# Kernel tuning notes

Hardware: AMD Instinct MI355X
Metric: run time of the kernel (lower is better)

The kernel has to match this reference:

```python
import jax, jax.numpy as jnp
import numpy as np

NUM_INPUTS = 1024
NUM_HIDDEN = 1024
FORGET_GATE_BIAS = -1.0
EPS = 1e-5


def layer_norm_1d(x, weight, bias):
    # Matches torch LayerNorm1D: std is unbiased (ddof=1), divide by (std + eps)
    mean = jnp.mean(x, axis=1, keepdims=True)
    std = jnp.std(x, axis=1, keepdims=True, ddof=1)
    return (x - mean) / (std + EPS) * weight + bias


def setup_inputs() -> dict:
    key = jax.random.key(0)
    ks = jax.random.split(key, 8)
    B, I, H = 4096, NUM_INPUTS, NUM_HIDDEN
    lim_i = 1.0 / np.sqrt(I)
    lim_h = 1.0 / np.sqrt(H)
    return {
        "inputs": jax.random.normal(ks[0], (B, I), jnp.float32),
        "hx": jax.random.normal(ks[1], (B, H), jnp.float32),
        "cx": jax.random.normal(ks[2], (B, H), jnp.float32),
        "w_i2h": jax.random.uniform(ks[3], (4 * H, I), jnp.float32, -lim_i, lim_i),
        "b_i2h": jax.random.uniform(ks[4], (4 * H,), jnp.float32, -lim_i, lim_i),
        "w_h2h": jax.random.uniform(ks[5], (4 * H, H), jnp.float32, -lim_h, lim_h),
        "b_h2h": jax.random.uniform(ks[6], (4 * H,), jnp.float32, -lim_h, lim_h),
        "ln_i2h_w": jnp.ones((1, 4 * H), jnp.float32),
        "ln_i2h_b": jnp.zeros((1, 4 * H), jnp.float32),
        "ln_h2h_w": jnp.ones((1, 4 * H), jnp.float32),
        "ln_h2h_b": jnp.zeros((1, 4 * H), jnp.float32),
        "ln_h2o_w": jnp.ones((1, H), jnp.float32),
        "ln_h2o_b": jnp.zeros((1, H), jnp.float32),
    }


def reference(inputs, hx, cx, w_i2h, b_i2h, w_h2h, b_h2h,
              ln_i2h_w, ln_i2h_b, ln_h2h_w, ln_h2h_b, ln_h2o_w, ln_h2o_b):
    H = NUM_HIDDEN
    i2h = inputs @ w_i2h.T + b_i2h          # [B, 4H]
    h2h = hx @ w_h2h.T + b_h2h              # [B, 4H]
    x = layer_norm_1d(i2h, ln_i2h_w, ln_i2h_b) + layer_norm_1d(h2h, ln_h2h_w, ln_h2h_b)
    g_i, g_f, g_o, g_c = jnp.split(x, 4, axis=1)
    in_gate = jax.nn.sigmoid(g_i)
    forget_gate = jax.nn.sigmoid(g_f + FORGET_GATE_BIAS)
    out_gate = jax.nn.sigmoid(g_o)
    in_transform = jnp.tanh(g_c)
    cx_new = forget_gate * cx + in_gate * in_transform
    hx_new = out_gate * jnp.tanh(layer_norm_1d(cx_new, ln_h2o_w, ln_h2o_b))
    return hx_new, cx_new
```

## Files before the change

### kernel.cpp

```cpp
#include <hip/hip_runtime.h>
#include <hip/hip_bf16.h>
#include <math.h>

#define NI 1024
#define NH 1024
#define H4 4096
#define FGB (-1.0f)
#define LN_EPS 1e-5f
#define NKT 32

typedef unsigned short u16;
typedef __attribute__((ext_vector_type(8))) short short8;
typedef __attribute__((ext_vector_type(8))) unsigned short ushort8v;
typedef __attribute__((ext_vector_type(16))) float f32x16;

__device__ __forceinline__ float bf2f(u16 u) {
    union { unsigned int i; float f; } v; v.i = ((unsigned int)u) << 16; return v.f;
}
__device__ __forceinline__ u16 f2bf(float f) {
    __hip_bfloat16 h = __float2bfloat16(f);
    return __builtin_bit_cast(u16, h);
}
__device__ __forceinline__ float fast_sigmoid(float x) {
    return 1.0f / (1.0f + __expf(-x));
}
__device__ __forceinline__ float fast_tanh(float x) {
    return 1.0f - 2.0f / (__expf(2.0f * x) + 1.0f);
}

__device__ __forceinline__ void gload16(const u16* g, u16* l) {
    __builtin_amdgcn_global_load_lds(
        (const __attribute__((address_space(1))) void*)g,
        (__attribute__((address_space(3))) void*)l,
        16, 0, 0);
}

__global__ __launch_bounds__(256) void shuffle_cast(
    const float* __restrict__ a, const float* __restrict__ b,
    const float* __restrict__ c, const float* __restrict__ d,
    u16* __restrict__ oa, u16* __restrict__ ob,
    u16* __restrict__ oc, u16* __restrict__ od)
{
    __shared__ u16 sT[32][264];

    const int my = blockIdx.y;
    const float* src = (my == 0) ? a : (my == 1) ? b : (my == 2) ? c : d;
    u16*         dst = (my == 0) ? oa : (my == 1) ? ob : (my == 2) ? oc : od;

    const int mtile = blockIdx.x >> 2;
    const int slab  = blockIdx.x & 3;
    const int t     = threadIdx.x;
    const int w     = t >> 6;
    const int lane  = t & 63;

    const float* s0 = src + (size_t)(mtile * 32) * 1024 + slab * 256 + lane * 4;
#pragma unroll
    for (int i = 0; i < 8; ++i) {
        const int row = i * 4 + w;
        float4 v = *(const float4*)(s0 + (size_t)row * 1024);
        ushort4 pk;
        pk.x = f2bf(v.x); pk.y = f2bf(v.y); pk.z = f2bf(v.z); pk.w = f2bf(v.w);
        *(ushort4*)&sT[row][lane * 4] = pk;
    }
    __syncthreads();

    const int r  = lane & 31;
    const int hi = lane >> 5;
#pragma unroll
    for (int j = 0; j < 2; ++j) {
        const int ktl = w * 2 + j;
        const int kt  = slab * 8 + ktl;
        u16* o = dst + ((size_t)(mtile * 32 + kt)) * 1024 + lane * 8;
#pragma unroll
        for (int kh = 0; kh < 2; ++kh) {
            ushort8v vv = *(const ushort8v*)&sT[r][ktl * 32 + kh * 16 + hi * 8];
            *(ushort8v*)(o + kh * 512) = vv;
        }
    }
}

__global__ __launch_bounds__(512, 2) void gemm_lds(
    const u16* __restrict__ Af0, const u16* __restrict__ Wf0,
    const float* __restrict__ bias0, u16* __restrict__ C0,
    const u16* __restrict__ Af1, const u16* __restrict__ Wf1,
    const float* __restrict__ bias1, u16* __restrict__ C1,
    int N)
{
    const u16*   Af   = blockIdx.z ? Af1 : Af0;
    const u16*   Wf   = blockIdx.z ? Wf1 : Wf0;
    const float* bias = blockIdx.z ? bias1 : bias0;
    u16*         C    = blockIdx.z ? C1 : C0;

    __shared__ __align__(16) u16 sA[4][8][2][512];
    __shared__ __align__(16) u16 sB[4][8][2][512];

    const int tid  = threadIdx.x;
    const int lane = tid & 63;
    const int wave = tid >> 6;
    const int wm   = wave >> 2;
    const int wn   = wave & 3;

    const u16* gA = Af + (size_t)(blockIdx.y * 8 + wave) * 32768 + lane * 8;
    const u16* gB = Wf + (size_t)(blockIdx.x * 8 + wave) * 32768 + lane * 8;

    f32x16 acc[4][2];
#pragma unroll
    for (int i = 0; i < 4; ++i)
#pragma unroll
        for (int j = 0; j < 2; ++j)
#pragma unroll
            for (int r = 0; r < 16; ++r)
                acc[i][j][r] = 0.f;

#define STAGE_A(kt)                                                          \
    do {                                                                     \
        gload16(gA + (size_t)(kt) * 1024,       &sA[(kt) & 3][wave][0][0]);  \
        gload16(gA + (size_t)(kt) * 1024 + 512, &sA[(kt) & 3][wave][1][0]);  \
    } while (0)
#define STAGE_B(kt)                                                          \
    do {                                                                     \
        gload16(gB + (size_t)(kt) * 1024,       &sB[(kt) & 3][wave][0][0]);  \
        gload16(gB + (size_t)(kt) * 1024 + 512, &sB[(kt) & 3][wave][1][0]);  \
    } while (0)

    ushort8v a00, a10, a20, a30, a01, a11, a21, a31;
    ushort8v b00, b10, b01, b11;

#define READS(slot)                                                          \
    do {                                                                     \
        a00 = *(const ushort8v*)&sA[slot][wm * 4 + 0][0][lane * 8];          \
        b00 = *(const ushort8v*)&sB[slot][wn * 2 + 0][0][lane * 8];          \
        a10 = *(const ushort8v*)&sA[slot][wm * 4 + 1][0][lane * 8];          \
        b10 = *(const ushort8v*)&sB[slot][wn * 2 + 1][0][lane * 8];          \
        a20 = *(const ushort8v*)&sA[slot][wm * 4 + 2][0][lane * 8];          \
        a30 = *(const ushort8v*)&sA[slot][wm * 4 + 3][0][lane * 8];          \
        a01 = *(const ushort8v*)&sA[slot][wm * 4 + 0][1][lane * 8];          \
        b01 = *(const ushort8v*)&sB[slot][wn * 2 + 0][1][lane * 8];          \
        a11 = *(const ushort8v*)&sA[slot][wm * 4 + 1][1][lane * 8];          \
        b11 = *(const ushort8v*)&sB[slot][wn * 2 + 1][1][lane * 8];          \
        a21 = *(const ushort8v*)&sA[slot][wm * 4 + 2][1][lane * 8];          \
        a31 = *(const ushort8v*)&sA[slot][wm * 4 + 3][1][lane * 8];          \
    } while (0)

#define MFMAS()                                                                                        \
    do {                                                                                               \
        acc[0][0] = __builtin_amdgcn_mfma_f32_32x32x16_bf16((short8)a00, (short8)b00, acc[0][0], 0, 0, 0); \
        acc[1][0] = __builtin_amdgcn_mfma_f32_32x32x16_bf16((short8)a10, (short8)b00, acc[1][0], 0, 0, 0); \
        acc[0][1] = __builtin_amdgcn_mfma_f32_32x32x16_bf16((short8)a00, (short8)b10, acc[0][1], 0, 0, 0); \
        acc[1][1] = __builtin_amdgcn_mfma_f32_32x32x16_bf16((short8)a10, (short8)b10, acc[1][1], 0, 0, 0); \
        acc[2][0] = __builtin_amdgcn_mfma_f32_32x32x16_bf16((short8)a20, (short8)b00, acc[2][0], 0, 0, 0); \
        acc[3][0] = __builtin_amdgcn_mfma_f32_32x32x16_bf16((short8)a30, (short8)b00, acc[3][0], 0, 0, 0); \
        acc[2][1] = __builtin_amdgcn_mfma_f32_32x32x16_bf16((short8)a20, (short8)b10, acc[2][1], 0, 0, 0); \
        acc[3][1] = __builtin_amdgcn_mfma_f32_32x32x16_bf16((short8)a30, (short8)b10, acc[3][1], 0, 0, 0); \
        acc[0][0] = __builtin_amdgcn_mfma_f32_32x32x16_bf16((short8)a01, (short8)b01, acc[0][0], 0, 0, 0); \
        acc[1][0] = __builtin_amdgcn_mfma_f32_32x32x16_bf16((short8)a11, (short8)b01, acc[1][0], 0, 0, 0); \
        acc[0][1] = __builtin_amdgcn_mfma_f32_32x32x16_bf16((short8)a01, (short8)b11, acc[0][1], 0, 0, 0); \
        acc[1][1] = __builtin_amdgcn_mfma_f32_32x32x16_bf16((short8)a11, (short8)b11, acc[1][1], 0, 0, 0); \
        acc[2][0] = __builtin_amdgcn_mfma_f32_32x32x16_bf16((short8)a21, (short8)b01, acc[2][0], 0, 0, 0); \
        acc[3][0] = __builtin_amdgcn_mfma_f32_32x32x16_bf16((short8)a31, (short8)b01, acc[3][0], 0, 0, 0); \
        acc[2][1] = __builtin_amdgcn_mfma_f32_32x32x16_bf16((short8)a21, (short8)b11, acc[2][1], 0, 0, 0); \
        acc[3][1] = __builtin_amdgcn_mfma_f32_32x32x16_bf16((short8)a31, (short8)b11, acc[3][1], 0, 0, 0); \
    } while (0)

#define KT_STEP(kt, slot, VM, DO_STAGE)                                      \
    do {                                                                     \
        asm volatile("s_waitcnt vmcnt(" VM ")" ::: "memory");                \
        __builtin_amdgcn_s_barrier();                                        \
        asm volatile("" ::: "memory");                                       \
        if (DO_STAGE) { STAGE_A((kt) + 3); STAGE_B((kt) + 3); }              \
        READS(slot);                                                         \
        __builtin_amdgcn_s_setprio(1);                                       \
        MFMAS();                                                             \
        __builtin_amdgcn_s_setprio(0);                                       \
    } while (0)

    STAGE_A(0); STAGE_B(0);
    STAGE_A(1); STAGE_B(1);
    STAGE_A(2); STAGE_B(2);

#pragma unroll
    for (int kt = 0; kt < NKT - 4; kt += 4) {
        KT_STEP(kt + 0, 0, "8", true);
        KT_STEP(kt + 1, 1, "8", true);
        KT_STEP(kt + 2, 2, "8", true);
        KT_STEP(kt + 3, 3, "8", true);
    }
    KT_STEP(NKT - 4, 0, "8", true);
    KT_STEP(NKT - 3, 1, "8", false);
    KT_STEP(NKT - 2, 2, "4", false);
    KT_STEP(NKT - 1, 3, "0", false);

#undef STAGE_A
#undef STAGE_B
#undef READS
#undef MFMAS
#undef KT_STEP

    const int m0  = blockIdx.y * 256;
    const int n0  = blockIdx.x * 256;
    const int l31 = lane & 31;
    float bv[2];
#pragma unroll
    for (int tn = 0; tn < 2; ++tn)
        bv[tn] = bias[n0 + wn * 64 + tn * 32 + l31];

    const int rbase = (lane >> 5) * 4;
#pragma unroll
    for (int tm = 0; tm < 4; ++tm)
#pragma unroll
        for (int reg = 0; reg < 16; ++reg) {
            const int row = m0 + wm * 128 + tm * 32 + (reg & 3) + 8 * (reg >> 2) + rbase;
#pragma unroll
            for (int tn = 0; tn < 2; ++tn) {
                const int col = n0 + wn * 64 + tn * 32 + l31;
                C[(size_t)row * N + col] = f2bf(acc[tm][tn][reg] + bv[tn]);
            }
        }
}

__global__ __launch_bounds__(256) void lstm_pointwise(
    const u16* __restrict__ i2h, const u16* __restrict__ h2h,
    const float* __restrict__ cx,
    const float* __restrict__ lwx, const float* __restrict__ lbx,
    const float* __restrict__ lwy, const float* __restrict__ lby,
    const float* __restrict__ lwc, const float* __restrict__ lbc,
    float* __restrict__ hx_out, float* __restrict__ cx_out)
{
    __shared__ u16 sX[H4];
    __shared__ u16 sY[H4];
    __shared__ float red[16];

    const int row  = blockIdx.x;
    const int tid  = threadIdx.x;
    const int lane = tid & 63;
    const int wid  = tid >> 6;

    const u16* xr = i2h + (size_t)row * H4;
    const u16* yr = h2h + (size_t)row * H4;

    float sx = 0.f, sxx = 0.f, sy = 0.f, syy = 0.f;
#pragma unroll
    for (int s = 0; s < 2; ++s) {
        const int off = s * 2048 + tid * 8;
        ushort8v xv = *(const ushort8v*)(xr + off);
        ushort8v yv = *(const ushort8v*)(yr + off);
        *(ushort8v*)(sX + off) = xv;
        *(ushort8v*)(sY + off) = yv;
#pragma unroll
        for (int e = 0; e < 8; ++e) {
            float x = bf2f(xv[e]), y = bf2f(yv[e]);
            sx += x; sxx += x * x; sy += y; syy += y * y;
        }
    }
#pragma unroll
    for (int m = 32; m; m >>= 1) {
        sx  += __shfl_xor(sx,  m, 64);
        sxx += __shfl_xor(sxx, m, 64);
        sy  += __shfl_xor(sy,  m, 64);
        syy += __shfl_xor(syy, m, 64);
    }
    if (lane == 0) {
        red[wid] = sx; red[4 + wid] = sxx; red[8 + wid] = sy; red[12 + wid] = syy;
    }
    __syncthreads();
    const float tsx  = red[0] + red[1] + red[2] + red[3];
    const float tsxx = red[4] + red[5] + red[6] + red[7];
    const float tsy  = red[8] + red[9] + red[10] + red[11];
    const float tsyy = red[12] + red[13] + red[14] + red[15];
    __syncthreads();

    const float n1  = (float)H4;
    const float mx  = tsx / n1;
    const float ivx = 1.0f / (sqrtf(fmaxf((tsxx - tsx * tsx / n1) / (n1 - 1.f), 0.f)) + LN_EPS);
    const float my  = tsy / n1;
    const float ivy = 1.0f / (sqrtf(fmaxf((tsyy - tsy * tsy / n1) / (n1 - 1.f), 0.f)) + LN_EPS);

    const int j0 = tid * 4;
    float gate[4][4];
#pragma unroll
    for (int g = 0; g < 4; ++g) {
        ushort4 xv = *(const ushort4*)(sX + g * NH + j0);
        ushort4 yv = *(const ushort4*)(sY + g * NH + j0);
        float4 wxv = *(const float4*)(lwx + g * NH + j0);
        float4 bxv = *(const float4*)(lbx + g * NH + j0);
        float4 wyv = *(const float4*)(lwy + g * NH + j0);
        float4 byv = *(const float4*)(lby + g * NH + j0);
        gate[g][0] = (bf2f(xv.x) - mx) * ivx * wxv.x + bxv.x + (bf2f(yv.x) - my) * ivy * wyv.x + byv.x;
        gate[g][1] = (bf2f(xv.y) - mx) * ivx * wxv.y + bxv.y + (bf2f(yv.y) - my) * ivy * wyv.y + byv.y;
        gate[g][2] = (bf2f(xv.z) - mx) * ivx * wxv.z + bxv.z + (bf2f(yv.z) - my) * ivy * wyv.z + byv.z;
        gate[g][3] = (bf2f(xv.w) - mx) * ivx * wxv.w + bxv.w + (bf2f(yv.w) - my) * ivy * wyv.w + byv.w;
    }

    float4 cxv = *(const float4*)(cx + (size_t)row * NH + j0);
    const float cin[4] = {cxv.x, cxv.y, cxv.z, cxv.w};
    float cvl[4], og[4];
    float sc = 0.f, scc = 0.f;
#pragma unroll
    for (int e = 0; e < 4; ++e) {
        float ing = fast_sigmoid(gate[0][e]);
        float fg  = fast_sigmoid(gate[1][e] + FGB);
        og[e]     = fast_sigmoid(gate[2][e]);
        float tr  = fast_tanh(gate[3][e]);
        float c   = fg * cin[e] + ing * tr;
        cvl[e] = c; sc += c; scc += c * c;
    }
    *(float4*)(cx_out + (size_t)row * NH + j0) = make_float4(cvl[0], cvl[1], cvl[2], cvl[3]);

#pragma unroll
    for (int m = 32; m; m >>= 1) {
        sc  += __shfl_xor(sc,  m, 64);
        scc += __shfl_xor(scc, m, 64);
    }
    if (lane == 0) { red[wid] = sc; red[4 + wid] = scc; }
    __syncthreads();
    const float tsc  = red[0] + red[1] + red[2] + red[3];
    const float tscc = red[4] + red[5] + red[6] + red[7];

    const float nc  = (float)NH;
    const float mc  = tsc / nc;
    const float ivc = 1.0f / (sqrtf(fmaxf((tscc - tsc * tsc / nc) / (nc - 1.f), 0.f)) + LN_EPS);

    float4 wcv = *(const float4*)(lwc + j0);
    float4 bcv = *(const float4*)(lbc + j0);
    float h0 = og[0] * fast_tanh((cvl[0] - mc) * ivc * wcv.x + bcv.x);
    float h1 = og[1] * fast_tanh((cvl[1] - mc) * ivc * wcv.y + bcv.y);
    float h2 = og[2] * fast_tanh((cvl[2] - mc) * ivc * wcv.z + bcv.z);
    float h3 = og[3] * fast_tanh((cvl[3] - mc) * ivc * wcv.w + bcv.w);
    *(float4*)(hx_out + (size_t)row * NH + j0) = make_float4(h0, h1, h2, h3);
}

extern "C" void kernel_launch(void* const* d_in, const int* in_sizes, int n_in,
                              void* d_out, int out_size, void* d_ws, size_t ws_size,
                              hipStream_t stream) {
    const float* inputs = (const float*)d_in[0];
    const float* hx     = (const float*)d_in[1];
    const float* cx     = (const float*)d_in[2];
    const float* w_i2h  = (const float*)d_in[3];
    const float* b_i2h  = (const float*)d_in[4];
    const float* w_h2h  = (const float*)d_in[5];
    const float* b_h2h  = (const float*)d_in[6];
    const float* lwx    = (const float*)d_in[7];
    const float* lbx    = (const float*)d_in[8];
    const float* lwy    = (const float*)d_in[9];
    const float* lby    = (const float*)d_in[10];
    const float* lwc    = (const float*)d_in[11];
    const float* lbc    = (const float*)d_in[12];

    const int B = in_sizes[0] / NI;

    u16* a_fr   = (u16*)d_ws;
    u16* hx_fr  = a_fr   + (size_t)B * NI;
    u16* wi_fr  = hx_fr  + (size_t)B * NH;
    u16* wh_fr  = wi_fr  + (size_t)H4 * NI;
    u16* i2h_bf = wh_fr  + (size_t)H4 * NH;
    u16* h2h_bf = i2h_bf + (size_t)B * H4;

    float* hx_out = (float*)d_out;
    float* cx_out = hx_out + (size_t)B * NH;

    shuffle_cast<<<dim3(512, 4), dim3(256), 0, stream>>>(
        inputs, hx, w_i2h, w_h2h, a_fr, hx_fr, wi_fr, wh_fr);

    gemm_lds<<<dim3(H4 / 256, B / 256, 2), dim3(512), 0, stream>>>(
        a_fr, wi_fr, b_i2h, i2h_bf,
        hx_fr, wh_fr, b_h2h, h2h_bf,
        H4);

    lstm_pointwise<<<dim3(B), dim3(256), 0, stream>>>(
        i2h_bf, h2h_bf, cx, lwx, lbx, lwy, lby, lwc, lbc, hx_out, cx_out);
}
```

Baseline: 243.9 us.

## Software-pipeline LDS reads against MFMAs and shorten global prefetch depth

```diff
diff --git a/kernel.cpp b/kernel.cpp
--- a/kernel.cpp
+++ b/kernel.cpp
@@ -112,89 +112,92 @@
             for (int r = 0; r < 16; ++r)
                 acc[i][j][r] = 0.f;
 
-#define STAGE_A(kt)                                                          \
+#define STAGE(kt)                                                            \
     do {                                                                     \
         gload16(gA + (size_t)(kt) * 1024,       &sA[(kt) & 3][wave][0][0]);  \
         gload16(gA + (size_t)(kt) * 1024 + 512, &sA[(kt) & 3][wave][1][0]);  \
-    } while (0)
-#define STAGE_B(kt)                                                          \
-    do {                                                                     \
         gload16(gB + (size_t)(kt) * 1024,       &sB[(kt) & 3][wave][0][0]);  \
         gload16(gB + (size_t)(kt) * 1024 + 512, &sB[(kt) & 3][wave][1][0]);  \
     } while (0)
 
-    ushort8v a00, a10, a20, a30, a01, a11, a21, a31;
-    ushort8v b00, b10, b01, b11;
-
-#define READS(slot)                                                          \
+    ushort8v a0_0, a1_0, a2_0, a3_0, b0_0, b1_0;
+    ushort8v a0_1, a1_1, a2_1, a3_1, b0_1, b1_1;
+
+#define R0(slot)                                                             \
     do {                                                                     \
-        a00 = *(const ushort8v*)&sA[slot][wm * 4 + 0][0][lane * 8];          \
-        b00 = *(const ushort8v*)&sB[slot][wn * 2 + 0][0][lane * 8];          \
-        a10 = *(const ushort8v*)&sA[slot][wm * 4 + 1][0][lane * 8];          \
-        b10 = *(const ushort8v*)&sB[slot][wn * 2 + 1][0][lane * 8];          \
-        a20 = *(const ushort8v*)&sA[slot][wm * 4 + 2][0][lane * 8];          \
-        a30 = *(const ushort8v*)&sA[slot][wm * 4 + 3][0][lane * 8];          \
-        a01 = *(const ushort8v*)&sA[slot][wm * 4 + 0][1][lane * 8];          \
-        b01 = *(const ushort8v*)&sB[slot][wn * 2 + 0][1][lane * 8];          \
-        a11 = *(const ushort8v*)&sA[slot][wm * 4 + 1][1][lane * 8];          \
-        b11 = *(const ushort8v*)&sB[slot][wn * 2 + 1][1][lane * 8];          \
-        a21 = *(const ushort8v*)&sA[slot][wm * 4 + 2][1][lane * 8];          \
-        a31 = *(const ushort8v*)&sA[slot][wm * 4 + 3][1][lane * 8];          \
+        a0_0 = *(const ushort8v*)&sA[slot][wm * 4 + 0][0][lane * 8];         \
+        a1_0 = *(const ushort8v*)&sA[slot][wm * 4 + 1][0][lane * 8];         \
+        b0_0 = *(const ushort8v*)&sB[slot][wn * 2 + 0][0][lane * 8];         \
+        b1_0 = *(const ushort8v*)&sB[slot][wn * 2 + 1][0][lane * 8];         \
+        a2_0 = *(const ushort8v*)&sA[slot][wm * 4 + 2][0][lane * 8];         \
+        a3_0 = *(const ushort8v*)&sA[slot][wm * 4 + 3][0][lane * 8];         \
     } while (0)
-
-#define MFMAS()                                                                                        \
-    do {                                                                                               \
-        acc[0][0] = __builtin_amdgcn_mfma_f32_32x32x16_bf16((short8)a00, (short8)b00, acc[0][0], 0, 0, 0); \
-        acc[1][0] = __builtin_amdgcn_mfma_f32_32x32x16_bf16((short8)a10, (short8)b00, acc[1][0], 0, 0, 0); \
-        acc[0][1] = __builtin_amdgcn_mfma_f32_32x32x16_bf16((short8)a00, (short8)b10, acc[0][1], 0, 0, 0); \
-        acc[1][1] = __builtin_amdgcn_mfma_f32_32x32x16_bf16((short8)a10, (short8)b10, acc[1][1], 0, 0, 0); \
-        acc[2][0] = __builtin_amdgcn_mfma_f32_32x32x16_bf16((short8)a20, (short8)b00, acc[2][0], 0, 0, 0); \
-        acc[3][0] = __builtin_amdgcn_mfma_f32_32x32x16_bf16((short8)a30, (short8)b00, acc[3][0], 0, 0, 0); \
-        acc[2][1] = __builtin_amdgcn_mfma_f32_32x32x16_bf16((short8)a20, (short8)b10, acc[2][1], 0, 0, 0); \
-        acc[3][1] = __builtin_amdgcn_mfma_f32_32x32x16_bf16((short8)a30, (short8)b10, acc[3][1], 0, 0, 0); \
-        acc[0][0] = __builtin_amdgcn_mfma_f32_32x32x16_bf16((short8)a01, (short8)b01, acc[0][0], 0, 0, 0); \
-        acc[1][0] = __builtin_amdgcn_mfma_f32_32x32x16_bf16((short8)a11, (short8)b01, acc[1][0], 0, 0, 0); \
-        acc[0][1] = __builtin_amdgcn_mfma_f32_32x32x16_bf16((short8)a01, (short8)b11, acc[0][1], 0, 0, 0); \
-        acc[1][1] = __builtin_amdgcn_mfma_f32_32x32x16_bf16((short8)a11, (short8)b11, acc[1][1], 0, 0, 0); \
-        acc[2][0] = __builtin_amdgcn_mfma_f32_32x32x16_bf16((short8)a21, (short8)b01, acc[2][0], 0, 0, 0); \
-        acc[3][0] = __builtin_amdgcn_mfma_f32_32x32x16_bf16((short8)a31, (short8)b01, acc[3][0], 0, 0, 0); \
-        acc[2][1] = __builtin_amdgcn_mfma_f32_32x32x16_bf16((short8)a21, (short8)b11, acc[2][1], 0, 0, 0); \
-        acc[3][1] = __builtin_amdgcn_mfma_f32_32x32x16_bf16((short8)a31, (short8)b11, acc[3][1], 0, 0, 0); \
+#define R1(slot)                                                             \
+    do {                                                                     \
+        a0_1 = *(const ushort8v*)&sA[slot][wm * 4 + 0][1][lane * 8];         \
+        a1_1 = *(const ushort8v*)&sA[slot][wm * 4 + 1][1][lane * 8];         \
+        b0_1 = *(const ushort8v*)&sB[slot][wn * 2 + 0][1][lane * 8];         \
+        b1_1 = *(const ushort8v*)&sB[slot][wn * 2 + 1][1][lane * 8];         \
+        a2_1 = *(const ushort8v*)&sA[slot][wm * 4 + 2][1][lane * 8];         \
+        a3_1 = *(const ushort8v*)&sA[slot][wm * 4 + 3][1][lane * 8];         \
     } while (0)
 
-#define KT_STEP(kt, slot, VM, DO_STAGE)                                      \
-    do {                                                                     \
-        asm volatile("s_waitcnt vmcnt(" VM ")" ::: "memory");                \
-        __builtin_amdgcn_s_barrier();                                        \
-        asm volatile("" ::: "memory");                                       \
-        if (DO_STAGE) { STAGE_A((kt) + 3); STAGE_B((kt) + 3); }              \
-        READS(slot);                                                         \
-        __builtin_amdgcn_s_setprio(1);                                       \
-        MFMAS();                                                             \
-        __builtin_amdgcn_s_setprio(0);                                       \
+#define M8(aa0, aa1, aa2, aa3, bb0, bb1)                                                             \
+    do {                                                                                             \
+        __builtin_amdgcn_s_setprio(1);                                                               \
+        acc[0][0] = __builtin_amdgcn_mfma_f32_32x32x16_bf16((short8)aa0, (short8)bb0, acc[0][0], 0, 0, 0); \
+        acc[1][0] = __builtin_amdgcn_mfma_f32_32x32x16_bf16((short8)aa1, (short8)bb0, acc[1][0], 0, 0, 0); \
+        acc[0][1] = __builtin_amdgcn_mfma_f32_32x32x16_bf16((short8)aa0, (short8)bb1, acc[0][1], 0, 0, 0); \
+        acc[1][1] = __builtin_amdgcn_mfma_f32_32x32x16_bf16((short8)aa1, (short8)bb1, acc[1][1], 0, 0, 0); \
+        acc[2][0] = __builtin_amdgcn_mfma_f32_32x32x16_bf16((short8)aa2, (short8)bb0, acc[2][0], 0, 0, 0); \
+        acc[3][0] = __builtin_amdgcn_mfma_f32_32x32x16_bf16((short8)aa3, (short8)bb0, acc[3][0], 0, 0, 0); \
+        acc[2][1] = __builtin_amdgcn_mfma_f32_32x32x16_bf16((short8)aa2, (short8)bb1, acc[2][1], 0, 0, 0); \
+        acc[3][1] = __builtin_amdgcn_mfma_f32_32x32x16_bf16((short8)aa3, (short8)bb1, acc[3][1], 0, 0, 0); \
+        __builtin_amdgcn_s_setprio(0);                                                               \
     } while (0)
 
-    STAGE_A(0); STAGE_B(0);
-    STAGE_A(1); STAGE_B(1);
-    STAGE_A(2); STAGE_B(2);
-
-#pragma unroll
-    for (int kt = 0; kt < NKT - 4; kt += 4) {
-        KT_STEP(kt + 0, 0, "8", true);
-        KT_STEP(kt + 1, 1, "8", true);
-        KT_STEP(kt + 2, 2, "8", true);
-        KT_STEP(kt + 3, 3, "8", true);
-    }
-    KT_STEP(NKT - 4, 0, "8", true);
-    KT_STEP(NKT - 3, 1, "8", false);
-    KT_STEP(NKT - 2, 2, "4", false);
-    KT_STEP(NKT - 1, 3, "0", false);
-
-#undef STAGE_A
-#undef STAGE_B
-#undef READS
-#undef MFMAS
-#undef KT_STEP
+#define M8_SET0() M8(a0_0, a1_0, a2_0, a3_0, b0_0, b1_0)
+#define M8_SET1() M8(a0_1, a1_1, a2_1, a3_1, b0_1, b1_1)
+
+#define FENCE() asm volatile("" ::: "memory")
+
+    STAGE(0);
+    STAGE(1);
+    asm volatile("s_waitcnt vmcnt(4)" ::: "memory");
+    FENCE();
+    __builtin_amdgcn_s_barrier();
+    FENCE();
+    STAGE(2);
+    R0(0);
+    R1(0);
+    M8_SET0();
+
+#pragma unroll
+    for (int kt = 1; kt < NKT; ++kt) {
+        const int slot = kt & 3;
+        if (kt == NKT - 1) {
+            asm volatile("s_waitcnt vmcnt(0)" ::: "memory");
+        } else {
+            asm volatile("s_waitcnt vmcnt(4)" ::: "memory");
+        }
+        FENCE();
+        __builtin_amdgcn_s_barrier();
+        FENCE();
+        if (kt + 2 < NKT) STAGE(kt + 2);
+        R0(slot);
+        M8_SET1();
+        R1(slot);
+        M8_SET0();
+    }
+    M8_SET1();
+
+#undef STAGE
+#undef R0
+#undef R1
+#undef M8
+#undef M8_SET0
+#undef M8_SET1
+#undef FENCE
 
     const int m0  = blockIdx.y * 256;
     const int n0  = blockIdx.x * 256;
```

Result: no change. 245.0 us (+0.5%).
